# Optimization experiments

Measured on AMD Instinct MI355X. Metric: run time of the kernel, lower is better.

The kernel has to match this reference:

```python
import jax, jax.numpy as jnp
import numpy as np

IN_C = 256
OUT_C = 256
KQ_C = 256
HEADS = 8

def setup_inputs() -> dict:
    key = jax.random.key(0)
    kx, kq, kk, kv = jax.random.split(key, 4)
    N, T = 4, 2048
    x = jax.random.normal(kx, (N, IN_C, T), dtype=jnp.float32)
    # Conv1d(kernel_size=1, bias=False) weights: [out, in]
    s = 1.0 / np.sqrt(IN_C)
    Wq = jax.random.uniform(kq, (KQ_C, IN_C), dtype=jnp.float32, minval=-s, maxval=s)
    Wk = jax.random.uniform(kk, (KQ_C, IN_C), dtype=jnp.float32, minval=-s, maxval=s)
    Wv = jax.random.uniform(kv, (OUT_C, IN_C), dtype=jnp.float32, minval=-s, maxval=s)
    return {"x": x, "Wq": Wq, "Wk": Wk, "Wv": Wv}

def reference(x, Wq, Wk, Wv):
    N, C, T = x.shape
    H = HEADS
    dk = KQ_C // H   # head dim for q/k
    dv = OUT_C // H  # head dim for v
    # 1x1 conv == channel matmul: [N,C,T] -> [N,out,T]
    q = jnp.einsum('oc,nct->not', Wq, x).reshape(N, H, dk, T)
    k = jnp.einsum('oc,nct->not', Wk, x).reshape(N, H, dk, T)
    v = jnp.einsum('oc,nct->not', Wv, x).reshape(N, H, dv, T)
    # scores: [N,H,T,T] = q^T k, scaled
    scores = jnp.einsum('nhdt,nhds->nhts', q, k) / np.sqrt(dk).astype(jnp.float32)
    attn = jax.nn.softmax(scores, axis=-1)
    # out: [N,H,T,dv] -> [N,H,dv,T] -> [N,OUT_C,T]
    out = jnp.einsum('nhts,nhds->nhdt', attn, v)
    return out.reshape(N, OUT_C, T)
```

## Files before the change

### kernel.cpp

```cpp
#include <hip/hip_runtime.h>


typedef float f32x4 __attribute__((ext_vector_type(4)));
typedef short short8 __attribute__((ext_vector_type(8)));
typedef short short4v __attribute__((ext_vector_type(4)));

#define WS_Q 0u
#define WS_K (4u << 20)
#define WS_V (8u << 20)
#define WS_X (12u << 20)
#define WS_W (16u << 20)
#define WS_OP (20u << 20)

__device__ __forceinline__ unsigned short f2bf(float f) {
  unsigned int u = __builtin_bit_cast(unsigned int, f);
  u += 0x7FFFu + ((u >> 16) & 1u);
  return (unsigned short)(u >> 16);
}

__device__ __forceinline__ int pack_bf16rn(float a, float b) {
  unsigned int ua = __builtin_bit_cast(unsigned int, a) + 0x8000u;
  unsigned int ub = __builtin_bit_cast(unsigned int, b) + 0x8000u;
  return __builtin_amdgcn_perm(ub, ua, 0x07060302);
}

__global__ __launch_bounds__(256) void pack_kernel(
    const float* __restrict__ x, const float* __restrict__ Wq,
    const float* __restrict__ Wk, const float* __restrict__ Wv,
    unsigned short* __restrict__ ws) {
  const int tid = threadIdx.x;
  const int lane = tid & 63;
  const int wv = tid >> 6;
  const int lc = lane & 15, lq = lane >> 4;
  const int b = blockIdx.x;
  alignas(16) unsigned short tmp[8];
  if (b < 1024) {
    const int r = b * 4 + wv;
    const int kc = r & 7, tt = (r >> 3) & 127, n = r >> 10;
    const int t = tt * 16 + lc;
    const int c0 = kc * 32 + lq * 8;
    const float* src = x + (size_t)(n * 256 + c0) * 2048 + t;
#pragma unroll
    for (int j = 0; j < 8; ++j) tmp[j] = f2bf(src[(size_t)j * 2048]);
    unsigned short* dst = ws + (WS_X >> 1) + (size_t)r * 512 + lane * 8;
    *(int4*)dst = *(const int4*)tmp;
  } else {
    const int r = (b - 1024) * 4 + wv;
    const int kc = r & 7, ot = (r >> 3) & 15, wi = r >> 7;
    const float* W = (wi == 0) ? Wq : (wi == 1) ? Wk : Wv;
    const float scale = (wi == 0) ? 0.25503492f : 1.0f;
    const int o = ot * 16 + lc;
    const int c0 = kc * 32 + lq * 8;
    const float* src = W + o * 256 + c0;
#pragma unroll
    for (int j = 0; j < 8; ++j) tmp[j] = f2bf(src[j] * scale);
    unsigned short* dst = ws + (WS_W >> 1) + (size_t)r * 512 + lane * 8;
    *(int4*)dst = *(const int4*)tmp;
  }
}

__global__ __launch_bounds__(256) void proj_kernel(unsigned short* __restrict__ ws) {
  __shared__ unsigned short eps[4][2048];
  const int tid = threadIdx.x, lane = tid & 63, w = tid >> 6;
  const int lc = lane & 15, lq = lane >> 4;
  const int tt2 = blockIdx.x;
  const int n = blockIdx.y;
  const int wi = blockIdx.z;
  const unsigned short* Xb = ws + (WS_X >> 1);
  const unsigned short* Wb = ws + (WS_W >> 1);

  short8 af[2][8];
#pragma unroll
  for (int mt = 0; mt < 2; ++mt)
#pragma unroll
    for (int kc = 0; kc < 8; ++kc)
      af[mt][kc] = *(const short8*)(Xb + ((size_t)((n * 128 + tt2 * 2 + mt) * 8 + kc) * 512 + lane * 8));

  f32x4 acc[2][4];
#pragma unroll
  for (int mt = 0; mt < 2; ++mt)
#pragma unroll
    for (int nt = 0; nt < 4; ++nt) {
      f32x4 z = {0.f, 0.f, 0.f, 0.f};
      acc[mt][nt] = z;
    }

#pragma unroll
  for (int kc = 0; kc < 8; ++kc) {
    short8 bf[4];
#pragma unroll
    for (int nt = 0; nt < 4; ++nt)
      bf[nt] = *(const short8*)(Wb + ((size_t)((wi * 16 + w * 4 + nt) * 8 + kc) * 512 + lane * 8));
#pragma unroll
    for (int mt = 0; mt < 2; ++mt)
#pragma unroll
      for (int nt = 0; nt < 4; ++nt)
        acc[mt][nt] = __builtin_amdgcn_mfma_f32_16x16x32_bf16(af[mt][kc], bf[nt], acc[mt][nt], 0, 0, 0);
  }

  if (wi < 2) {
    unsigned short* ep = eps[w];
#pragma unroll
    for (int mt = 0; mt < 2; ++mt)
#pragma unroll
      for (int nt = 0; nt < 4; ++nt) {
        const int m2 = ((nt & 1) << 1) | (lc >> 3);
        const int base = ((mt * 2 + (nt >> 1)) << 9) + (m2 << 7) + (lq << 5) + (lc & 7);
#pragma unroll
        for (int r = 0; r < 4; ++r)
          ep[base + ((r ^ m2) << 3)] = f2bf(acc[mt][nt][r]);
      }
    const int swzl = lane ^ (lane >> 4);
    unsigned short* dst = ws + ((wi == 0) ? (WS_Q >> 1) : (WS_K >> 1));
#pragma unroll
    for (int rl = 0; rl < 4; ++rl) {
      int4 v = *(const int4*)(ep + (rl << 9) + swzl * 8);
      const int mt = rl >> 1, hh = rl & 1;
      const int nh = n * 8 + w * 2 + hh;
      const int ttg = tt2 * 2 + mt;
      *(int4*)(dst + ((size_t)(nh * 128 + ttg) * 64 + lane) * 8) = v;
    }
  } else {
    const int kb = tt2 >> 1, sbp = tt2 & 1;
#pragma unroll
    for (int nt = 0; nt < 4; ++nt) {
      const int nh = n * 8 + w * 2 + (nt >> 1);
      const int dt = nt & 1;
      alignas(16) unsigned short tmp[8];
#pragma unroll
      for (int mt = 0; mt < 2; ++mt)
#pragma unroll
        for (int r = 0; r < 4; ++r) tmp[mt * 4 + r] = f2bf(acc[mt][nt][r]);
      unsigned short* dstv = ws + (WS_V >> 1) +
          ((size_t)((((nh * 32 + kb) * 2 + dt) * 2 + sbp)) * 64 + lane) * 8;
      *(int4*)dstv = *(const int4*)tmp;
    }
  }
}

template <int KS>
__global__ __launch_bounds__(128, 5) void attn_kernel(
    const unsigned short* __restrict__ ws, float* __restrict__ out,
    float* __restrict__ opart, float* __restrict__ lpart) {
  const int tid = threadIdx.x;
  const int lane = tid & 63, wv = tid >> 6;
  const int lc = lane & 15, quad = lane >> 4;
  const int qw = blockIdx.x * 2 + wv;
  const int nh = blockIdx.y;
  const int ks = blockIdx.z;
  constexpr int NKB = 32 / KS;
  const int kb0 = ks * NKB;

  const unsigned short* Qw = ws + (WS_Q >> 1) + ((size_t)(nh * 128 + qw * 2)) * 512;
  const unsigned short* Kb = ws + (WS_K >> 1) + (size_t)nh * 65536;
  const unsigned short* Vb = ws + (WS_V >> 1) + (size_t)nh * 65536;

  short8 qf[2];
  qf[0] = *(const short8*)(Qw + lane * 8);
  qf[1] = *(const short8*)(Qw + 512 + lane * 8);

  f32x4 acc[2][2];
#pragma unroll
  for (int mt = 0; mt < 2; ++mt)
#pragma unroll
    for (int dt = 0; dt < 2; ++dt) {
      f32x4 z = {0.f, 0.f, 0.f, 0.f};
      acc[mt][dt] = z;
    }
  float lsum[2] = {0.f, 0.f};

  for (int kb = kb0; kb < kb0 + NKB; ++kb) {
    const unsigned short* kp = Kb + (size_t)kb * 2048 + lane * 8;
    const unsigned short* vp = Vb + (size_t)kb * 2048 + lane * 8;
    short8 kf[4], vv[4];
#pragma unroll
    for (int sb = 0; sb < 4; ++sb) kf[sb] = *(const short8*)(kp + sb * 512);
#pragma unroll
    for (int u = 0; u < 4; ++u) vv[u] = *(const short8*)(vp + u * 512);

    short4v pf[2][4];
#pragma unroll
    for (int mt = 0; mt < 2; ++mt) {
      f32x4 st[4];
#pragma unroll
      for (int sb = 0; sb < 4; ++sb) {
        f32x4 z = {0.f, 0.f, 0.f, 0.f};
        st[sb] = __builtin_amdgcn_mfma_f32_16x16x32_bf16(kf[sb], qf[mt], z, 0, 0, 0);
      }
#pragma unroll
      for (int sb = 0; sb < 4; ++sb) {
        float p0 = __builtin_amdgcn_exp2f(st[sb][0]);
        float p1 = __builtin_amdgcn_exp2f(st[sb][1]);
        float p2 = __builtin_amdgcn_exp2f(st[sb][2]);
        float p3 = __builtin_amdgcn_exp2f(st[sb][3]);
        lsum[mt] += (p0 + p1) + (p2 + p3);
        int2 pi;
        pi.x = pack_bf16rn(p0, p1);
        pi.y = pack_bf16rn(p2, p3);
        pf[mt][sb] = __builtin_bit_cast(short4v, pi);
      }
    }

    short4v vf[4][2];
#pragma unroll
    for (int dt = 0; dt < 2; ++dt)
#pragma unroll
      for (int sbp = 0; sbp < 2; ++sbp) {
        short8 t = vv[dt * 2 + sbp];
        vf[sbp * 2 + 0][dt] = __builtin_shufflevector(t, t, 0, 1, 2, 3);
        vf[sbp * 2 + 1][dt] = __builtin_shufflevector(t, t, 4, 5, 6, 7);
      }
#pragma unroll
    for (int sb = 0; sb < 4; ++sb)
#pragma unroll
      for (int mt = 0; mt < 2; ++mt) {
        acc[mt][0] = __builtin_amdgcn_mfma_f32_16x16x16bf16_1k(pf[mt][sb], vf[sb][0], acc[mt][0], 0, 0, 0);
        acc[mt][1] = __builtin_amdgcn_mfma_f32_16x16x16bf16_1k(pf[mt][sb], vf[sb][1], acc[mt][1], 0, 0, 0);
      }
  }

#pragma unroll
  for (int mt = 0; mt < 2; ++mt) {
    lsum[mt] += __shfl_xor(lsum[mt], 16);
    lsum[mt] += __shfl_xor(lsum[mt], 32);
  }

  if constexpr (KS == 1) {
    const int chbase = (nh >> 3) * 256 + (nh & 7) * 32;
#pragma unroll
    for (int mt = 0; mt < 2; ++mt) {
      float is[4];
#pragma unroll
      for (int r = 0; r < 4; ++r) is[r] = 1.0f / __shfl(lsum[mt], quad * 4 + r);
      const int tb = qw * 32 + mt * 16 + quad * 4;
#pragma unroll
      for (int dt = 0; dt < 2; ++dt) {
        f32x4 ov;
#pragma unroll
        for (int r = 0; r < 4; ++r) ov[r] = acc[mt][dt][r] * is[r];
        *(f32x4*)(out + (size_t)(chbase + dt * 16 + lc) * 2048 + tb) = ov;
      }
    }
  } else {
    const size_t ob = (size_t)(ks * 32 + nh) * 32 * 2048;
#pragma unroll
    for (int mt = 0; mt < 2; ++mt) {
      const int tb = qw * 32 + mt * 16 + quad * 4;
#pragma unroll
      for (int dt = 0; dt < 2; ++dt)
        *(f32x4*)(opart + ob + (size_t)(dt * 16 + lc) * 2048 + tb) = acc[mt][dt];
      if (quad == 0)
        lpart[(size_t)(ks * 32 + nh) * 2048 + qw * 32 + mt * 16 + lc] = lsum[mt];
    }
  }
}

template <int KS>
__global__ __launch_bounds__(256) void finalize_kernel(
    const float* __restrict__ opart, const float* __restrict__ lpart,
    float* __restrict__ out) {
  const int f = blockIdx.x * 256 + threadIdx.x;
  const int t4 = f & 511;
  const int c = f >> 9;
  const int n = c >> 8, ch = c & 255;
  const int nh = n * 8 + (ch >> 5), d = ch & 31;
  float4 o = {0.f, 0.f, 0.f, 0.f}, l = {0.f, 0.f, 0.f, 0.f};
#pragma unroll
  for (int ks = 0; ks < KS; ++ks) {
    const float4 ov = *(const float4*)(opart + ((size_t)(ks * 32 + nh) * 32 + d) * 2048 + t4 * 4);
    const float4 lv = *(const float4*)(lpart + (size_t)(ks * 32 + nh) * 2048 + t4 * 4);
    o.x += ov.x; o.y += ov.y; o.z += ov.z; o.w += ov.w;
    l.x += lv.x; l.y += lv.y; l.z += lv.z; l.w += lv.w;
  }
  float4 r;
  r.x = o.x / l.x; r.y = o.y / l.y; r.z = o.z / l.z; r.w = o.w / l.w;
  *(float4*)(out + (size_t)f * 4) = r;
}

extern "C" void kernel_launch(void* const* d_in, const int* in_sizes, int n_in,
                              void* d_out, int out_size, void* d_ws, size_t ws_size,
                              hipStream_t stream) {
  const float* x = (const float*)d_in[0];
  const float* Wq = (const float*)d_in[1];
  const float* Wk = (const float*)d_in[2];
  const float* Wv = (const float*)d_in[3];
  unsigned short* ws = (unsigned short*)d_ws;
  float* out = (float*)d_out;
  (void)in_sizes; (void)n_in; (void)out_size;

  pack_kernel<<<1120, 256, 0, stream>>>(x, Wq, Wk, Wv, ws);
  proj_kernel<<<dim3(64, 4, 3), 256, 0, stream>>>(ws);

  char* wsb = (char*)d_ws;
  float* opart = (float*)(wsb + WS_OP);
  if (ws_size >= ((size_t)54u << 20)) {
    float* lpart = (float*)(wsb + WS_OP + ((size_t)4 * 8u << 20));
    attn_kernel<4><<<dim3(32, 32, 4), 128, 0, stream>>>(ws, out, opart, lpart);
    finalize_kernel<4><<<2048, 256, 0, stream>>>(opart, lpart, out);
  } else if (ws_size >= ((size_t)38u << 20)) {
    float* lpart = (float*)(wsb + WS_OP + ((size_t)2 * 8u << 20));
    attn_kernel<2><<<dim3(32, 32, 2), 128, 0, stream>>>(ws, out, opart, lpart);
    finalize_kernel<2><<<2048, 256, 0, stream>>>(opart, lpart, out);
  } else {
    attn_kernel<1><<<dim3(32, 32, 1), 128, 0, stream>>>(ws, out, nullptr, nullptr);
  }
}
```

Baseline: 111.7 us.

## Stage K/V blocks in double-buffered LDS shared by four waves per block

```diff
diff --git a/kernel.cpp b/kernel.cpp
--- a/kernel.cpp
+++ b/kernel.cpp
@@ -139,26 +139,30 @@
 }
 
 template <int KS>
-__global__ __launch_bounds__(128, 5) void attn_kernel(
+__global__ __launch_bounds__(256, 6) void attn_kernel(
     const unsigned short* __restrict__ ws, float* __restrict__ out,
     float* __restrict__ opart, float* __restrict__ lpart) {
+  __shared__ __align__(16) char smem[16384];
   const int tid = threadIdx.x;
   const int lane = tid & 63, wv = tid >> 6;
   const int lc = lane & 15, quad = lane >> 4;
-  const int qw = blockIdx.x * 2 + wv;
+  const int qw = blockIdx.x * 4 + wv;
   const int nh = blockIdx.y;
   const int ks = blockIdx.z;
   constexpr int NKB = 32 / KS;
-  const int kb0 = ks * NKB;
 
   const unsigned short* Qw = ws + (WS_Q >> 1) + ((size_t)(nh * 128 + qw * 2)) * 512;
-  const unsigned short* Kb = ws + (WS_K >> 1) + (size_t)nh * 65536;
-  const unsigned short* Vb = ws + (WS_V >> 1) + (size_t)nh * 65536;
+  const char* Kc = (const char*)ws + WS_K + (size_t)nh * 131072 + (size_t)(ks * NKB) * 4096;
+  const char* Vc = (const char*)ws + WS_V + (size_t)nh * 131072 + (size_t)(ks * NKB) * 4096;
 
   short8 qf[2];
   qf[0] = *(const short8*)(Qw + lane * 8);
   qf[1] = *(const short8*)(Qw + 512 + lane * 8);
 
+  *(int4*)(smem + tid * 16) = *(const int4*)(Kc + tid * 16);
+  *(int4*)(smem + 4096 + tid * 16) = *(const int4*)(Vc + tid * 16);
+  __syncthreads();
+
   f32x4 acc[2][2];
 #pragma unroll
   for (int mt = 0; mt < 2; ++mt)
@@ -169,14 +173,21 @@
     }
   float lsum[2] = {0.f, 0.f};
 
-  for (int kb = kb0; kb < kb0 + NKB; ++kb) {
-    const unsigned short* kp = Kb + (size_t)kb * 2048 + lane * 8;
-    const unsigned short* vp = Vb + (size_t)kb * 2048 + lane * 8;
-    short8 kf[4], vv[4];
-#pragma unroll
-    for (int sb = 0; sb < 4; ++sb) kf[sb] = *(const short8*)(kp + sb * 512);
-#pragma unroll
-    for (int u = 0; u < 4; ++u) vv[u] = *(const short8*)(vp + u * 512);
+  for (int it = 0; it < NKB; ++it) {
+    int4 pk, pv;
+    const bool pre = (it + 1 < NKB);
+    if (pre) {
+      pk = *(const int4*)(Kc + (it + 1) * 4096 + tid * 16);
+      pv = *(const int4*)(Vc + (it + 1) * 4096 + tid * 16);
+    }
+    const unsigned short* kb = (const unsigned short*)(smem + (it & 1) * 8192);
+    const unsigned short* vb = kb + 2048;
+
+    short8 kf[4], vvr[4];
+#pragma unroll
+    for (int sb = 0; sb < 4; ++sb) kf[sb] = *(const short8*)(kb + sb * 512 + lane * 8);
+#pragma unroll
+    for (int u = 0; u < 4; ++u) vvr[u] = *(const short8*)(vb + u * 512 + lane * 8);
 
     short4v pf[2][4];
 #pragma unroll
@@ -206,7 +217,7 @@
     for (int dt = 0; dt < 2; ++dt)
 #pragma unroll
       for (int sbp = 0; sbp < 2; ++sbp) {
-        short8 t = vv[dt * 2 + sbp];
+        short8 t = vvr[dt * 2 + sbp];
         vf[sbp * 2 + 0][dt] = __builtin_shufflevector(t, t, 0, 1, 2, 3);
         vf[sbp * 2 + 1][dt] = __builtin_shufflevector(t, t, 4, 5, 6, 7);
       }
@@ -217,6 +228,13 @@
         acc[mt][0] = __builtin_amdgcn_mfma_f32_16x16x16bf16_1k(pf[mt][sb], vf[sb][0], acc[mt][0], 0, 0, 0);
         acc[mt][1] = __builtin_amdgcn_mfma_f32_16x16x16bf16_1k(pf[mt][sb], vf[sb][1], acc[mt][1], 0, 0, 0);
       }
+
+    if (pre) {
+      char* db = smem + ((it + 1) & 1) * 8192;
+      *(int4*)(db + tid * 16) = pk;
+      *(int4*)(db + 4096 + tid * 16) = pv;
+    }
+    __syncthreads();
   }
 
 #pragma unroll
@@ -295,13 +313,13 @@
   float* opart = (float*)(wsb + WS_OP);
   if (ws_size >= ((size_t)54u << 20)) {
     float* lpart = (float*)(wsb + WS_OP + ((size_t)4 * 8u << 20));
-    attn_kernel<4><<<dim3(32, 32, 4), 128, 0, stream>>>(ws, out, opart, lpart);
+    attn_kernel<4><<<dim3(16, 32, 4), 256, 0, stream>>>(ws, out, opart, lpart);
     finalize_kernel<4><<<2048, 256, 0, stream>>>(opart, lpart, out);
   } else if (ws_size >= ((size_t)38u << 20)) {
     float* lpart = (float*)(wsb + WS_OP + ((size_t)2 * 8u << 20));
-    attn_kernel<2><<<dim3(32, 32, 2), 128, 0, stream>>>(ws, out, opart, lpart);
+    attn_kernel<2><<<dim3(16, 32, 2), 256, 0, stream>>>(ws, out, opart, lpart);
     finalize_kernel<2><<<2048, 256, 0, stream>>>(opart, lpart, out);
   } else {
-    attn_kernel<1><<<dim3(32, 32, 1), 128, 0, stream>>>(ws, out, nullptr, nullptr);
-  }
-}
+    attn_kernel<1><<<dim3(16, 32, 1), 256, 0, stream>>>(ws, out, nullptr, nullptr);
+  }
+}
```

Result: slower. 181.7 us (+62.7%).

## Store split-K attention partials as bf16 and flatten grid for head-major block order

Applied to the files above, without the earlier changes.

```diff
diff --git a/kernel.cpp b/kernel.cpp
--- a/kernel.cpp
+++ b/kernel.cpp
@@ -141,13 +141,16 @@
 template <int KS>
 __global__ __launch_bounds__(128, 5) void attn_kernel(
     const unsigned short* __restrict__ ws, float* __restrict__ out,
-    float* __restrict__ opart, float* __restrict__ lpart) {
+    unsigned short* __restrict__ opart, float* __restrict__ lpart) {
   const int tid = threadIdx.x;
   const int lane = tid & 63, wv = tid >> 6;
   const int lc = lane & 15, quad = lane >> 4;
-  const int qw = blockIdx.x * 2 + wv;
-  const int nh = blockIdx.y;
-  const int ks = blockIdx.z;
+  constexpr int CH = 32 * KS;
+  const int c = blockIdx.x & (CH - 1);
+  const int qx = blockIdx.x / CH;
+  const int nh = c & 31;
+  const int ks = c >> 5;
+  const int qw = qx * 2 + wv;
   constexpr int NKB = 32 / KS;
   const int kb0 = ks * NKB;
 
@@ -172,11 +175,11 @@
   for (int kb = kb0; kb < kb0 + NKB; ++kb) {
     const unsigned short* kp = Kb + (size_t)kb * 2048 + lane * 8;
     const unsigned short* vp = Vb + (size_t)kb * 2048 + lane * 8;
-    short8 kf[4], vv[4];
+    short8 kf[4], vvr[4];
 #pragma unroll
     for (int sb = 0; sb < 4; ++sb) kf[sb] = *(const short8*)(kp + sb * 512);
 #pragma unroll
-    for (int u = 0; u < 4; ++u) vv[u] = *(const short8*)(vp + u * 512);
+    for (int u = 0; u < 4; ++u) vvr[u] = *(const short8*)(vp + u * 512);
 
     short4v pf[2][4];
 #pragma unroll
@@ -206,7 +209,7 @@
     for (int dt = 0; dt < 2; ++dt)
 #pragma unroll
       for (int sbp = 0; sbp < 2; ++sbp) {
-        short8 t = vv[dt * 2 + sbp];
+        short8 t = vvr[dt * 2 + sbp];
         vf[sbp * 2 + 0][dt] = __builtin_shufflevector(t, t, 0, 1, 2, 3);
         vf[sbp * 2 + 1][dt] = __builtin_shufflevector(t, t, 4, 5, 6, 7);
       }
@@ -247,8 +250,12 @@
     for (int mt = 0; mt < 2; ++mt) {
       const int tb = qw * 32 + mt * 16 + quad * 4;
 #pragma unroll
-      for (int dt = 0; dt < 2; ++dt)
-        *(f32x4*)(opart + ob + (size_t)(dt * 16 + lc) * 2048 + tb) = acc[mt][dt];
+      for (int dt = 0; dt < 2; ++dt) {
+        int2 pi;
+        pi.x = pack_bf16rn(acc[mt][dt][0], acc[mt][dt][1]);
+        pi.y = pack_bf16rn(acc[mt][dt][2], acc[mt][dt][3]);
+        *(int2*)(opart + ob + (size_t)(dt * 16 + lc) * 2048 + tb) = pi;
+      }
       if (quad == 0)
         lpart[(size_t)(ks * 32 + nh) * 2048 + qw * 32 + mt * 16 + lc] = lsum[mt];
     }
@@ -257,23 +264,28 @@
 
 template <int KS>
 __global__ __launch_bounds__(256) void finalize_kernel(
-    const float* __restrict__ opart, const float* __restrict__ lpart,
+    const unsigned short* __restrict__ opart, const float* __restrict__ lpart,
     float* __restrict__ out) {
   const int f = blockIdx.x * 256 + threadIdx.x;
   const int t4 = f & 511;
   const int c = f >> 9;
   const int n = c >> 8, ch = c & 255;
   const int nh = n * 8 + (ch >> 5), d = ch & 31;
-  float4 o = {0.f, 0.f, 0.f, 0.f}, l = {0.f, 0.f, 0.f, 0.f};
+  float o[4] = {0.f, 0.f, 0.f, 0.f};
+  float l[4] = {0.f, 0.f, 0.f, 0.f};
 #pragma unroll
   for (int ks = 0; ks < KS; ++ks) {
-    const float4 ov = *(const float4*)(opart + ((size_t)(ks * 32 + nh) * 32 + d) * 2048 + t4 * 4);
+    const short4v ov = *(const short4v*)(opart + ((size_t)(ks * 32 + nh) * 32 + d) * 2048 + t4 * 4);
     const float4 lv = *(const float4*)(lpart + (size_t)(ks * 32 + nh) * 2048 + t4 * 4);
-    o.x += ov.x; o.y += ov.y; o.z += ov.z; o.w += ov.w;
-    l.x += lv.x; l.y += lv.y; l.z += lv.z; l.w += lv.w;
+#pragma unroll
+    for (int i = 0; i < 4; ++i) {
+      const unsigned int u = ((unsigned int)(unsigned short)ov[i]) << 16;
+      o[i] += __builtin_bit_cast(float, u);
+    }
+    l[0] += lv.x; l[1] += lv.y; l[2] += lv.z; l[3] += lv.w;
   }
   float4 r;
-  r.x = o.x / l.x; r.y = o.y / l.y; r.z = o.z / l.z; r.w = o.w / l.w;
+  r.x = o[0] / l[0]; r.y = o[1] / l[1]; r.z = o[2] / l[2]; r.w = o[3] / l[3];
   *(float4*)(out + (size_t)f * 4) = r;
 }
 
@@ -292,16 +304,16 @@
   proj_kernel<<<dim3(64, 4, 3), 256, 0, stream>>>(ws);
 
   char* wsb = (char*)d_ws;
-  float* opart = (float*)(wsb + WS_OP);
-  if (ws_size >= ((size_t)54u << 20)) {
-    float* lpart = (float*)(wsb + WS_OP + ((size_t)4 * 8u << 20));
-    attn_kernel<4><<<dim3(32, 32, 4), 128, 0, stream>>>(ws, out, opart, lpart);
+  unsigned short* opart = (unsigned short*)(wsb + WS_OP);
+  if (ws_size >= ((size_t)41u << 20)) {
+    float* lpart = (float*)(wsb + WS_OP + ((size_t)4 * 4u << 20));
+    attn_kernel<4><<<4096, 128, 0, stream>>>(ws, out, opart, lpart);
     finalize_kernel<4><<<2048, 256, 0, stream>>>(opart, lpart, out);
-  } else if (ws_size >= ((size_t)38u << 20)) {
-    float* lpart = (float*)(wsb + WS_OP + ((size_t)2 * 8u << 20));
-    attn_kernel<2><<<dim3(32, 32, 2), 128, 0, stream>>>(ws, out, opart, lpart);
+  } else if (ws_size >= ((size_t)30u << 20)) {
+    float* lpart = (float*)(wsb + WS_OP + ((size_t)2 * 4u << 20));
+    attn_kernel<2><<<2048, 128, 0, stream>>>(ws, out, opart, lpart);
     finalize_kernel<2><<<2048, 256, 0, stream>>>(opart, lpart, out);
   } else {
-    attn_kernel<1><<<dim3(32, 32, 1), 128, 0, stream>>>(ws, out, nullptr, nullptr);
-  }
-}
+    attn_kernel<1><<<1024, 128, 0, stream>>>(ws, out, nullptr, nullptr);
+  }
+}
```

Result: no change. 111.7 us, median of 2 (+0.0%).
